# Kernel optimization log

Hardware: AMD Instinct MI355X
Metric: run time of the kernel (lower is better)

The kernel has to match this reference:

```python
import math
import jax, jax.numpy as jnp
import numpy as np

HIDDEN = 768
N_SIGNALS = 15
DIM = HIDDEN // 4  # 192
B, S = 32, 4096


def setup_inputs() -> dict:
    key = jax.random.key(0)
    ks = jax.random.split(key, 11)
    return {
        "token_embeds": jax.random.normal(ks[0], (B, S, HIDDEN), jnp.float32),
        "Wk": jax.random.normal(ks[1], (HIDDEN, DIM), jnp.float32) * 0.02,
        "bk": jax.random.normal(ks[2], (DIM,), jnp.float32) * 0.02,
        "Wv": jax.random.normal(ks[3], (HIDDEN, DIM), jnp.float32) * 0.02,
        "bv": jax.random.normal(ks[4], (DIM,), jnp.float32) * 0.02,
        "signal_queries": jax.random.normal(ks[5], (N_SIGNALS, DIM), jnp.float32),
        "null_embeddings": jax.random.normal(ks[6], (N_SIGNALS, HIDDEN), jnp.float32) * 0.01,
        "W1": jax.random.normal(ks[7], (2 * DIM, 64), jnp.float32) * 0.05,
        "b1": jax.random.normal(ks[8], (64,), jnp.float32) * 0.05,
        "W2": jax.random.normal(ks[9], (64, 1), jnp.float32) * 0.05,
        "b2": jax.random.normal(ks[10], (1,), jnp.float32) * 0.05,
    }


def reference(token_embeds, Wk, bk, Wv, bv, signal_queries, null_embeddings, W1, b1, W2, b2):
    b, s, h = token_embeds.shape
    d = Wk.shape[1]
    # detect_signals: cross-attention from signal queries to tokens
    keys = token_embeds @ Wk + bk        # [B,S,d]
    values = token_embeds @ Wv + bv      # [B,S,d]
    scale = jnp.sqrt(jnp.float32(d))
    attn = jnp.einsum("nd,bsd->bns", signal_queries, keys) / scale  # [B,N,S]
    attn_weights = jax.nn.softmax(attn, axis=-1)
    signal_embeds = jnp.einsum("bns,bsd->bnd", attn_weights, values)  # [B,N,d]
    entropy = -(attn_weights * jnp.log(attn_weights + 1e-10)).sum(-1)  # [B,N]
    strength = 1.0 - entropy / jnp.float32(math.log(s))
    # estimate_causal_effects: batched over the 15 signals (original loops in Python)
    null_proj = jnp.broadcast_to(null_embeddings[:, :d], (b, null_embeddings.shape[0], d))
    eff_in = jnp.concatenate([signal_embeds, null_proj], axis=-1)  # [B,N,2d]
    hdn = jax.nn.gelu(eff_in @ W1 + b1, approximate=False)
    effects = (hdn @ W2 + b2)[..., 0]  # [B,N]
    # package (effects, strength) as one array [B, 2N]
    return jnp.concatenate([effects, strength], axis=-1)
```

## Files before the change

kernel.cpp:

```cpp
#include <hip/hip_runtime.h>
#include <math.h>

#define HID   768
#define DIMD  192
#define NSIG  15
#define BB    32
#define SS    4096
#define SC    128
#define NCHUNK (SS / SC)
#define HC2   16
#define NST   (192 / HC2)
#define INV_SCALE 0.07216878364870322f
#define LOG_S     8.31776616671934f

#define WS_QK   ((size_t)0)
#define WS_QB   (WS_QK + NSIG * HID)
#define WS_ST   (WS_QB + 16)
#define WS_CTXP (WS_ST + (size_t)BB * NCHUNK * NSIG * 3)

__global__ __launch_bounds__(256) void k_qk(const float* __restrict__ q,
                                            const float* __restrict__ Wk,
                                            const float* __restrict__ bk,
                                            float* __restrict__ ws) {
  int idx = blockIdx.x * 256 + threadIdx.x;
  if (idx < NSIG * HID) {
    int n = idx / HID, h = idx - n * HID;
    const float* qr = q + n * DIMD;
    const float* wr = Wk + h * DIMD;
    float s = 0.f;
    #pragma unroll 4
    for (int d = 0; d < DIMD; ++d) s = fmaf(qr[d], wr[d], s);
    ws[WS_QK + (size_t)n * HID + h] = s * INV_SCALE;
  }
  if (idx < NSIG) {
    const float* qr = q + idx * DIMD;
    float s = 0.f;
    for (int d = 0; d < DIMD; ++d) s = fmaf(qr[d], bk[d], s);
    ws[WS_QB + idx] = s * INV_SCALE;
  }
}

__global__ __launch_bounds__(512, 8) void k_fused(const float* __restrict__ X,
                                                  const float* __restrict__ qk,
                                                  const float* __restrict__ qb,
                                                  float* __restrict__ stats,
                                                  float* __restrict__ ctxp) {
  __shared__ float smem[4 * SC * 17];
  const int t = threadIdx.x;
  const int chunk = blockIdx.x, b = blockIdx.y;
  const int tk = t & (SC - 1);
  const int q  = __builtin_amdgcn_readfirstlane(t >> 7);
  const float* Xb = X + ((size_t)(b * SS + chunk * SC)) * HID;

  float4 r[4];
  #pragma unroll
  for (int m = 0; m < 4; ++m) {
    int j = t + m * 512;
    int c4 = j & 3, row = (j >> 2) & (SC - 1), qq = j >> 9;
    r[m] = *(const float4*)(Xb + (size_t)row * HID + qq * DIMD + c4 * 4);
  }

  float acc[NSIG];
  #pragma unroll
  for (int n = 0; n < NSIG; ++n) acc[n] = (q == 0) ? qb[n] : 0.f;

  for (int c = 0; c < NST; ++c) {
    __syncthreads();
    #pragma unroll
    for (int m = 0; m < 4; ++m) {
      int j = t + m * 512;
      int c4 = j & 3, row = (j >> 2) & (SC - 1), qq = j >> 9;
      float* dst = smem + (qq * SC + row) * 17 + c4 * 4;
      dst[0] = r[m].x; dst[1] = r[m].y; dst[2] = r[m].z; dst[3] = r[m].w;
    }
    __syncthreads();
    if (c + 1 < NST) {
      #pragma unroll
      for (int m = 0; m < 4; ++m) {
        int j = t + m * 512;
        int c4 = j & 3, row = (j >> 2) & (SC - 1), qq = j >> 9;
        r[m] = *(const float4*)(Xb + (size_t)row * HID + qq * DIMD + (c + 1) * HC2 + c4 * 4);
      }
    }
    const float* xrow = smem + (q * SC + tk) * 17;
    float x[HC2];
    #pragma unroll
    for (int j = 0; j < HC2; ++j) x[j] = xrow[j];
    const float* Qc = qk + q * DIMD + c * HC2;
    #pragma unroll
    for (int n = 0; n < NSIG; ++n) {
      const float* Qn = Qc + (size_t)n * HID;
      float s = 0.f;
      #pragma unroll
      for (int j = 0; j < HC2; ++j) s = fmaf(x[j], Qn[j], s);
      acc[n] += s;
    }
  }

  __syncthreads();
  float* comb = smem;
  float* redM = smem + 3 * NSIG * SC;
  float* redL = redM + NSIG * 2;
  float* redP = redL + NSIG * 2;
  float* wS   = smem + 3 * NSIG * SC + 96;
  const int wv = __builtin_amdgcn_readfirstlane((t >> 6) & 1);

  if (q != 0) {
    #pragma unroll
    for (int n = 0; n < NSIG; ++n) comb[((q - 1) * NSIG + n) * SC + tk] = acc[n];
  }
  if (t >= 384) wS[NSIG * SC + (t - 384)] = 0.f;
  __syncthreads();
  if (q == 0) {
    #pragma unroll
    for (int n = 0; n < NSIG; ++n) {
      acc[n] += comb[n * SC + tk] + comb[(NSIG + n) * SC + tk] + comb[(2 * NSIG + n) * SC + tk];
      float v = acc[n];
      #pragma unroll
      for (int o = 32; o > 0; o >>= 1) v = fmaxf(v, __shfl_xor(v, o, 64));
      if ((t & 63) == 0) redM[n * 2 + wv] = v;
    }
  }
  __syncthreads();
  if (q == 0) {
    #pragma unroll
    for (int n = 0; n < NSIG; ++n) {
      float m = fmaxf(redM[n * 2], redM[n * 2 + 1]);
      float e = expf(acc[n] - m);
      wS[n * SC + tk] = e;
      float l = e, pa = e * acc[n];
      #pragma unroll
      for (int o = 32; o > 0; o >>= 1) { l += __shfl_xor(l, o, 64); pa += __shfl_xor(pa, o, 64); }
      if ((t & 63) == 0) { redL[n * 2 + wv] = l; redP[n * 2 + wv] = pa; }
    }
  }
  __syncthreads();
  if (t < NSIG) {
    float m  = fmaxf(redM[t * 2], redM[t * 2 + 1]);
    float l  = redL[t * 2] + redL[t * 2 + 1];
    float pa = redP[t * 2] + redP[t * 2 + 1];
    float* st = stats + ((size_t)((b * NCHUNK + chunk) * NSIG + t)) * 3;
    st[0] = m; st[1] = l; st[2] = pa;
  }

  const int cc = t & 255;
  const int nh = __builtin_amdgcn_readfirstlane(t >> 8);
  const int n0 = nh * 8;
  float accB[24];
  #pragma unroll
  for (int i = 0; i < 24; ++i) accB[i] = 0.f;
  const float* Xc = Xb + cc;
  for (int s = 0; s < SC; s += 4) {
    float x[12];
    #pragma unroll
    for (int j = 0; j < 4; ++j)
      #pragma unroll
      for (int k = 0; k < 3; ++k)
        x[j * 3 + k] = Xc[(size_t)(s + j) * HID + k * 256];
    #pragma unroll
    for (int i = 0; i < 8; ++i) {
      float4 w4 = *(const float4*)(wS + (n0 + i) * SC + s);
      float wa[4] = {w4.x, w4.y, w4.z, w4.w};
      #pragma unroll
      for (int j = 0; j < 4; ++j)
        #pragma unroll
        for (int k = 0; k < 3; ++k)
          accB[i * 3 + k] = fmaf(wa[j], x[j * 3 + k], accB[i * 3 + k]);
    }
  }
  float* dst = ctxp + ((size_t)((b * NCHUNK + chunk) * NSIG)) * HID + cc;
  #pragma unroll
  for (int i = 0; i < 8; ++i)
    if (n0 + i < NSIG)
      #pragma unroll
      for (int k = 0; k < 3; ++k)
        dst[(size_t)(n0 + i) * HID + k * 256] = accB[i * 3 + k];
}

__global__ __launch_bounds__(256) void k_final(const float* __restrict__ stats,
                                               const float* __restrict__ ctxp,
                                               const float* __restrict__ Wv,
                                               const float* __restrict__ bv,
                                               const float* __restrict__ nullemb,
                                               const float* __restrict__ W1,
                                               const float* __restrict__ b1,
                                               const float* __restrict__ W2,
                                               const float* __restrict__ b2,
                                               float* __restrict__ out) {
  const int blk = blockIdx.x;
  const int b = blk / NSIG, n = blk - b * NSIG;
  const int t = threadIdx.x;
  __shared__ float alpha[NCHUNK];
  __shared__ float ctx[HID];
  __shared__ float se[DIMD];

  if (t == 0) {
    float mc[NCHUNK], lc[NCHUNK], pc[NCHUNK];
    float m = -1e30f;
    #pragma unroll
    for (int c = 0; c < NCHUNK; ++c) {
      const float* st = stats + ((size_t)((b * NCHUNK + c) * NSIG + n)) * 3;
      mc[c] = st[0]; lc[c] = st[1]; pc[c] = st[2];
      m = fmaxf(m, mc[c]);
    }
    float L = 0.f, PA = 0.f;
    #pragma unroll
    for (int c = 0; c < NCHUNK; ++c) {
      float scl = expf(mc[c] - m);
      L = fmaf(scl, lc[c], L); PA = fmaf(scl, pc[c], PA);
    }
    #pragma unroll
    for (int c = 0; c < NCHUNK; ++c) alpha[c] = expf(mc[c] - m) / L;
    float entropy = m + logf(L) - PA / L;
    out[b * (2 * NSIG) + NSIG + n] = 1.f - entropy / LOG_S;
  }
  __syncthreads();

  #pragma unroll
  for (int k = 0; k < 3; ++k) {
    int h = t + k * 256;
    float s0 = 0.f, s1 = 0.f;
    #pragma unroll 8
    for (int c = 0; c < NCHUNK; c += 2) {
      s0 = fmaf(alpha[c],     ctxp[((size_t)((b * NCHUNK + c)     * NSIG + n)) * HID + h], s0);
      s1 = fmaf(alpha[c + 1], ctxp[((size_t)((b * NCHUNK + c + 1) * NSIG + n)) * HID + h], s1);
    }
    ctx[h] = s0 + s1;
  }
  __syncthreads();

  if (t < DIMD) {
    float s0 = 0.f, s1 = 0.f, s2 = 0.f, s3 = 0.f;
    #pragma unroll 2
    for (int h = 0; h < HID; h += 4) {
      s0 = fmaf(ctx[h],     Wv[(size_t)h       * DIMD + t], s0);
      s1 = fmaf(ctx[h + 1], Wv[(size_t)(h + 1) * DIMD + t], s1);
      s2 = fmaf(ctx[h + 2], Wv[(size_t)(h + 2) * DIMD + t], s2);
      s3 = fmaf(ctx[h + 3], Wv[(size_t)(h + 3) * DIMD + t], s3);
    }
    se[t] = bv[t] + ((s0 + s1) + (s2 + s3));
  }
  __syncthreads();

  if (t < 64) {
    float s0 = b1[t], s1 = 0.f, s2 = 0.f, s3 = 0.f;
    const float* nrow = nullemb + (size_t)n * HID;
    #pragma unroll 4
    for (int i = 0; i < DIMD; i += 2) {
      s0 = fmaf(se[i],     W1[(size_t)i       * 64 + t], s0);
      s1 = fmaf(se[i + 1], W1[(size_t)(i + 1) * 64 + t], s1);
    }
    #pragma unroll 4
    for (int i = 0; i < DIMD; i += 2) {
      s2 = fmaf(nrow[i],     W1[(size_t)(DIMD + i)     * 64 + t], s2);
      s3 = fmaf(nrow[i + 1], W1[(size_t)(DIMD + i + 1) * 64 + t], s3);
    }
    float s = (s0 + s1) + (s2 + s3);
    float g = 0.5f * s * (1.f + erff(s * 0.70710678118654752f));
    float val = g * W2[t];
    #pragma unroll
    for (int o = 32; o > 0; o >>= 1) val += __shfl_down(val, o, 64);
    if (t == 0) out[b * (2 * NSIG) + n] = val + b2[0];
  }
}

extern "C" void kernel_launch(void* const* d_in, const int* in_sizes, int n_in,
                              void* d_out, int out_size, void* d_ws, size_t ws_size,
                              hipStream_t stream) {
  const float* X   = (const float*)d_in[0];
  const float* Wk  = (const float*)d_in[1];
  const float* bk  = (const float*)d_in[2];
  const float* Wv  = (const float*)d_in[3];
  const float* bv  = (const float*)d_in[4];
  const float* q   = (const float*)d_in[5];
  const float* nul = (const float*)d_in[6];
  const float* W1  = (const float*)d_in[7];
  const float* b1  = (const float*)d_in[8];
  const float* W2  = (const float*)d_in[9];
  const float* b2  = (const float*)d_in[10];
  float* out = (float*)d_out;
  float* ws  = (float*)d_ws;

  hipLaunchKernelGGL(k_qk, dim3(45), dim3(256), 0, stream, q, Wk, bk, ws);
  hipLaunchKernelGGL(k_fused, dim3(NCHUNK, BB), dim3(512), 0, stream,
                     X, ws + WS_QK, ws + WS_QB, ws + WS_ST, ws + WS_CTXP);
  hipLaunchKernelGGL(k_final, dim3(BB * NSIG), dim3(256), 0, stream,
                     ws + WS_ST, ws + WS_CTXP, Wv, bv, nul, W1, b1, W2, b2, out);
}
```

Measured before the change: 736.0 us.

## Stage contiguous 64-column X tiles and parallelize chunk-stat merge across lanes

The fused scoring kernel now stages contiguous 64-float column slabs of each token row into LDS, instead of four separate 16-float pieces from each quarter of the hidden dimension. Each of the four thread groups takes a 16-column sub-slice of the staged slab, and the stage count drops from 12 to 12 with wider per-row reads. The aim is more coalesced global loads with longer contiguous segments per row. The final kernel also replaces the single-thread serial merge of 32 chunk statistics with a 32-lane shuffle reduction.

```diff
diff --git a/kernel.cpp b/kernel.cpp
--- a/kernel.cpp
+++ b/kernel.cpp
@@ -8,8 +8,10 @@
 #define SS    4096
 #define SC    128
 #define NCHUNK (SS / SC)
+#define CSTG  64
+#define NST   (HID / CSTG)
 #define HC2   16
-#define NST   (192 / HC2)
+#define LDSW  65
 #define INV_SCALE 0.07216878364870322f
 #define LOG_S     8.31776616671934f
 
@@ -45,48 +47,48 @@
                                                   const float* __restrict__ qb,
                                                   float* __restrict__ stats,
                                                   float* __restrict__ ctxp) {
-  __shared__ float smem[4 * SC * 17];
+  __shared__ float smem[SC * LDSW];
   const int t = threadIdx.x;
   const int chunk = blockIdx.x, b = blockIdx.y;
   const int tk = t & (SC - 1);
-  const int q  = __builtin_amdgcn_readfirstlane(t >> 7);
+  const int g  = __builtin_amdgcn_readfirstlane(t >> 7);
   const float* Xb = X + ((size_t)(b * SS + chunk * SC)) * HID;
 
   float4 r[4];
   #pragma unroll
   for (int m = 0; m < 4; ++m) {
-    int j = t + m * 512;
-    int c4 = j & 3, row = (j >> 2) & (SC - 1), qq = j >> 9;
-    r[m] = *(const float4*)(Xb + (size_t)row * HID + qq * DIMD + c4 * 4);
+    int idx = t + m * 512;
+    int c4 = idx & 15, row = idx >> 4;
+    r[m] = *(const float4*)(Xb + (size_t)row * HID + c4 * 4);
   }
 
   float acc[NSIG];
   #pragma unroll
-  for (int n = 0; n < NSIG; ++n) acc[n] = (q == 0) ? qb[n] : 0.f;
+  for (int n = 0; n < NSIG; ++n) acc[n] = (g == 0) ? qb[n] : 0.f;
 
   for (int c = 0; c < NST; ++c) {
     __syncthreads();
     #pragma unroll
     for (int m = 0; m < 4; ++m) {
-      int j = t + m * 512;
-      int c4 = j & 3, row = (j >> 2) & (SC - 1), qq = j >> 9;
-      float* dst = smem + (qq * SC + row) * 17 + c4 * 4;
+      int idx = t + m * 512;
+      int c4 = idx & 15, row = idx >> 4;
+      float* dst = smem + row * LDSW + c4 * 4;
       dst[0] = r[m].x; dst[1] = r[m].y; dst[2] = r[m].z; dst[3] = r[m].w;
     }
     __syncthreads();
     if (c + 1 < NST) {
       #pragma unroll
       for (int m = 0; m < 4; ++m) {
-        int j = t + m * 512;
-        int c4 = j & 3, row = (j >> 2) & (SC - 1), qq = j >> 9;
-        r[m] = *(const float4*)(Xb + (size_t)row * HID + qq * DIMD + (c + 1) * HC2 + c4 * 4);
+        int idx = t + m * 512;
+        int c4 = idx & 15, row = idx >> 4;
+        r[m] = *(const float4*)(Xb + (size_t)row * HID + (c + 1) * CSTG + c4 * 4);
       }
     }
-    const float* xrow = smem + (q * SC + tk) * 17;
+    const float* xrow = smem + tk * LDSW + g * HC2;
     float x[HC2];
     #pragma unroll
     for (int j = 0; j < HC2; ++j) x[j] = xrow[j];
-    const float* Qc = qk + q * DIMD + c * HC2;
+    const float* Qc = qk + c * CSTG + g * HC2;
     #pragma unroll
     for (int n = 0; n < NSIG; ++n) {
       const float* Qn = Qc + (size_t)n * HID;
@@ -105,13 +107,13 @@
   float* wS   = smem + 3 * NSIG * SC + 96;
   const int wv = __builtin_amdgcn_readfirstlane((t >> 6) & 1);
 
-  if (q != 0) {
-    #pragma unroll
-    for (int n = 0; n < NSIG; ++n) comb[((q - 1) * NSIG + n) * SC + tk] = acc[n];
+  if (g != 0) {
+    #pragma unroll
+    for (int n = 0; n < NSIG; ++n) comb[((g - 1) * NSIG + n) * SC + tk] = acc[n];
   }
   if (t >= 384) wS[NSIG * SC + (t - 384)] = 0.f;
   __syncthreads();
-  if (q == 0) {
+  if (g == 0) {
     #pragma unroll
     for (int n = 0; n < NSIG; ++n) {
       acc[n] += comb[n * SC + tk] + comb[(NSIG + n) * SC + tk] + comb[(2 * NSIG + n) * SC + tk];
@@ -122,7 +124,7 @@
     }
   }
   __syncthreads();
-  if (q == 0) {
+  if (g == 0) {
     #pragma unroll
     for (int n = 0; n < NSIG; ++n) {
       float m = fmaxf(redM[n * 2], redM[n * 2 + 1]);
@@ -194,25 +196,21 @@
   __shared__ float ctx[HID];
   __shared__ float se[DIMD];
 
-  if (t == 0) {
-    float mc[NCHUNK], lc[NCHUNK], pc[NCHUNK];
-    float m = -1e30f;
-    #pragma unroll
-    for (int c = 0; c < NCHUNK; ++c) {
-      const float* st = stats + ((size_t)((b * NCHUNK + c) * NSIG + n)) * 3;
-      mc[c] = st[0]; lc[c] = st[1]; pc[c] = st[2];
-      m = fmaxf(m, mc[c]);
-    }
-    float L = 0.f, PA = 0.f;
-    #pragma unroll
-    for (int c = 0; c < NCHUNK; ++c) {
-      float scl = expf(mc[c] - m);
-      L = fmaf(scl, lc[c], L); PA = fmaf(scl, pc[c], PA);
-    }
-    #pragma unroll
-    for (int c = 0; c < NCHUNK; ++c) alpha[c] = expf(mc[c] - m) / L;
-    float entropy = m + logf(L) - PA / L;
-    out[b * (2 * NSIG) + NSIG + n] = 1.f - entropy / LOG_S;
+  if (t < NCHUNK) {
+    const float* st = stats + ((size_t)((b * NCHUNK + t) * NSIG + n)) * 3;
+    float mc = st[0], lc = st[1], pc = st[2];
+    float m = mc;
+    #pragma unroll
+    for (int o = 16; o > 0; o >>= 1) m = fmaxf(m, __shfl_xor(m, o, 64));
+    float scl = expf(mc - m);
+    float L = scl * lc, PA = scl * pc;
+    #pragma unroll
+    for (int o = 16; o > 0; o >>= 1) { L += __shfl_xor(L, o, 64); PA += __shfl_xor(PA, o, 64); }
+    alpha[t] = scl / L;
+    if (t == 0) {
+      float entropy = m + logf(L) - PA / L;
+      out[b * (2 * NSIG) + NSIG + n] = 1.f - entropy / LOG_S;
+    }
   }
   __syncthreads();
 
```

New measurement: 712.8 us. -3.2%, faster.
